# Performance work log

Hardware: AMD Instinct MI355X
Metric: run time of the kernel (lower is better)

Reference implementation:

```python
import jax, jax.numpy as jnp
import numpy as np

N, D_TOK, K = 8192, 256, 16


def knn_idx(xyz, k):
    # squared pairwise distances, diagonal excluded (loop=False)
    sq = jnp.sum(xyz * xyz, axis=-1)                      # [N]
    dist = sq[:, None] - 2.0 * (xyz @ xyz.T) + sq[None, :]  # [N,N]
    dist = dist + jnp.eye(xyz.shape[0], dtype=xyz.dtype) * jnp.asarray(1e10, xyz.dtype)
    _, idx = jax.lax.top_k(-dist, k)                      # [N,k] nearest neighbors j for each target i
    return idx


def edgeconv(x, nbr, W1, b1, W2, b2):
    # EdgeConv message: nn(concat(x_i, x_j - x_i)), aggr = max over neighbors
    n, d = x.shape
    k = nbr.shape[1]
    xi = x[:, None, :]                                    # [N,1,D]
    xj = x[nbr]                                           # [N,k,D] gather
    msg = jnp.concatenate([jnp.broadcast_to(xi, (n, k, d)), xj - xi], axis=-1)  # [N,k,2D]
    h = jax.nn.relu(msg @ W1 + b1) @ W2 + b2              # [N,k,token_dim]
    return jnp.max(h, axis=1)                             # [N,token_dim]


def setup_inputs() -> dict:
    key = jax.random.key(0)
    ks = jax.random.split(key, 10)
    d_in = 2 * (D_TOK + 3)
    s1 = 1.0 / np.sqrt(d_in)
    s2 = 1.0 / np.sqrt(D_TOK)
    return {
        "xyz": jax.random.normal(ks[0], (N, 3), dtype=jnp.float32),
        "feat": jax.random.normal(ks[1], (N, D_TOK), dtype=jnp.float32),
        "W1a": jax.random.normal(ks[2], (d_in, D_TOK), dtype=jnp.float32) * s1,
        "b1a": jnp.zeros((D_TOK,), dtype=jnp.float32),
        "W2a": jax.random.normal(ks[3], (D_TOK, D_TOK), dtype=jnp.float32) * s2,
        "b2a": jnp.zeros((D_TOK,), dtype=jnp.float32),
        "W1b": jax.random.normal(ks[4], (d_in, D_TOK), dtype=jnp.float32) * s1,
        "b1b": jnp.zeros((D_TOK,), dtype=jnp.float32),
        "W2b": jax.random.normal(ks[5], (D_TOK, D_TOK), dtype=jnp.float32) * s2,
        "b2b": jnp.zeros((D_TOK,), dtype=jnp.float32),
    }


def reference(xyz, feat, W1a, b1a, W2a, b2a, W1b, b1b, W2b, b2b):
    nbr = knn_idx(xyz, K)                                 # [N,k], built once, reused by both convs
    x = jnp.concatenate([feat, xyz], axis=-1)             # [N, D_TOK+3]
    x = edgeconv(x, nbr, W1a, b1a, W2a, b2a)              # [N, D_TOK]
    x = jnp.concatenate([x, xyz], axis=-1)                # [N, D_TOK+3]
    x = edgeconv(x, nbr, W1b, b1b, W2b, b2b)              # [N, D_TOK]
    return x
```

## Files before the change

### kernel.cpp

```cpp
#include <hip/hip_runtime.h>
#include <cfloat>

#define N_PTS 8192
#define DTOK 256
#define KNN 16

typedef __attribute__((ext_vector_type(8))) short short8;
typedef __attribute__((ext_vector_type(4))) float float4v;

__device__ inline short f2bf(float f) {
  unsigned u = __float_as_uint(f);
  u += 0x7fffu + ((u >> 16) & 1u);
  return (short)(u >> 16);
}
__device__ inline float bf2f(short h) {
  return __uint_as_float(((unsigned)(unsigned short)h) << 16);
}

__global__ __launch_bounds__(256) void knn_prep_kernel(
    const float* __restrict__ xyz, float4* __restrict__ xyz4) {
  const int i = blockIdx.x * 256 + threadIdx.x;
  float x = xyz[3 * i], y = xyz[3 * i + 1], z = xyz[3 * i + 2];
  float sq = __fadd_rn(__fadd_rn(__fmul_rn(x, x), __fmul_rn(y, y)),
                       __fmul_rn(z, z));
  xyz4[i] = make_float4(x, y, z, sq);
}

__device__ inline float cand_dist(const float4 p, float xi, float yi, float zi,
                                  float sqi, int j, int i) {
  const float dot = fmaf(zi, p.z, fmaf(yi, p.y, __fmul_rn(xi, p.x)));
  float d = __fadd_rn(__fsub_rn(sqi, __fmul_rn(2.0f, dot)), p.w);
  if (j == i) d = __fadd_rn(d, 1e10f);
  return d;
}

__global__ __launch_bounds__(256) void knn_select_kernel(
    const float4* __restrict__ xyz4, int* __restrict__ nbr) {
  const int lane = threadIdx.x & 63;
  const int i = blockIdx.x * 4 + (threadIdx.x >> 6);

  const float4 pi = xyz4[i];
  const float xi = pi.x, yi = pi.y, zi = pi.z, sqi = pi.w;

  float lmin = FLT_MAX;
  #pragma unroll 4
  for (int base = 0; base < N_PTS; base += 64) {
    const int j = base + lane;
    const float4 p = xyz4[j];
    lmin = fminf(lmin, cand_dist(p, xi, yi, zi, sqi, j, i));
  }

  float v = lmin;
  #pragma unroll
  for (int k = 2; k <= 64; k <<= 1) {
    #pragma unroll
    for (int j = k >> 1; j > 0; j >>= 1) {
      const float o = __shfl_xor(v, j, 64);
      const bool up = ((lane & k) == 0);
      const bool lo = ((lane & j) == 0);
      v = (up == lo) ? fminf(v, o) : fmaxf(v, o);
    }
  }
  const float t = __shfl(v, 15, 64);

  float sd = FLT_MAX;
  int sj = 0;
  float s15 = FLT_MAX;

  for (int base = 0; base < N_PTS; base += 64) {
    const int j = base + lane;
    const float4 p = xyz4[j];
    const float d = cand_dist(p, xi, yi, zi, sqi, j, i);

    unsigned long long m = __ballot((d < s15) && (d <= t));
    while (m) {
      const int src = __ffsll(m) - 1;
      m &= m - 1;
      const float dc = __shfl(d, src);
      if (dc < s15) {
        const int jc = base + src;
        const unsigned long long bm = __ballot(sd <= dc) & 0xFFFFull;
        const int pos = (int)__popcll(bm);
        const float pu = __shfl_up(sd, 1);
        const int ju = __shfl_up(sj, 1);
        if (lane < 16) {
          if (lane > pos)        { sd = pu; sj = ju; }
          else if (lane == pos)  { sd = dc; sj = jc; }
        }
        s15 = __shfl(sd, 15);
      }
    }
  }
  if (lane < 16) nbr[i * KNN + lane] = sj;
}

__global__ __launch_bounds__(256) void convert_w_kernel(
    const float* __restrict__ W1, short* __restrict__ bhi,
    short* __restrict__ blo) {
  const int n = blockIdx.x;
  const int k = threadIdx.x;
  const float v = (n < 256) ? W1[k * DTOK + n]
                            : W1[(259 + k) * DTOK + (n - 256)];
  short h = f2bf(v);
  bhi[n * 256 + k] = h;
  blo[n * 256 + k] = f2bf(v - bf2f(h));
}

__global__ __launch_bounds__(256, 2) void pq_gemm_fused_kernel(
    const float* __restrict__ A, const short* __restrict__ Bthi,
    const short* __restrict__ Btlo, const float* __restrict__ xyz,
    const float* __restrict__ W1, const float* __restrict__ b1,
    float* __restrict__ R, float* __restrict__ Q) {
  __shared__ short Ahi[64][32], Alo[64][32];
  __shared__ short Bhi[128][32], Blo[128][32];
  __shared__ float Qs[64][65];
  __shared__ float sx[64][3];
  __shared__ float swz[6][64];
  __shared__ float sb1[64];

  const int tid = threadIdx.x;
  const int lane = tid & 63;
  const int wave = tid >> 6;
  const int l15 = lane & 15;
  const int quad = lane >> 4;
  const int mh = wave & 1;
  const int qh = wave >> 1;
  const int m0 = blockIdx.x * 64;
  const int np0 = blockIdx.y * 64;

  if (tid < 64) {
    sx[tid][0] = xyz[(m0 + tid) * 3];
    sx[tid][1] = xyz[(m0 + tid) * 3 + 1];
    sx[tid][2] = xyz[(m0 + tid) * 3 + 2];
  } else if (tid < 128) {
    int n = tid - 64;
    sb1[n] = b1[np0 + n];
    #pragma unroll
    for (int r = 0; r < 3; ++r) {
      swz[r][n] = W1[(256 + r) * DTOK + np0 + n];
      swz[3 + r][n] = W1[(515 + r) * DTOK + np0 + n];
    }
  }

  float4v acc[2][4];
  #pragma unroll
  for (int mf = 0; mf < 2; ++mf)
    #pragma unroll
    for (int nf = 0; nf < 4; ++nf)
      #pragma unroll
      for (int e = 0; e < 4; ++e) acc[mf][nf][e] = 0.f;

  const int ar = tid >> 2;
  const int ak = (tid & 3) * 8;

  #pragma unroll 1
  for (int kc = 0; kc < 8; ++kc) {
    const int k0 = kc * 32;
    __syncthreads();
    {
      const float* asrc = A + (size_t)(m0 + ar) * 256 + k0 + ak;
      float4 a0 = *(const float4*)asrc;
      float4 a1 = *(const float4*)(asrc + 4);
      float v[8] = {a0.x, a0.y, a0.z, a0.w, a1.x, a1.y, a1.z, a1.w};
      short8 h8, l8;
      #pragma unroll
      for (int e = 0; e < 8; ++e) {
        short h = f2bf(v[e]);
        h8[e] = h;
        l8[e] = f2bf(v[e] - bf2f(h));
      }
      *(short8*)(&Ahi[ar][ak]) = h8;
      *(short8*)(&Alo[ar][ak]) = l8;
    }
    #pragma unroll
    for (int l = 0; l < 4; ++l) {
      const int rem = tid + 256 * (l & 1);
      const int row = rem >> 2;
      const int koff = (rem & 3) * 8;
      const int n = (row < 64) ? (np0 + row) : (256 + np0 + row - 64);
      const short* src = ((l < 2) ? Bthi : Btlo) + (size_t)n * 256 + k0 + koff;
      short8 vv = *(const short8*)src;
      if (l < 2) *(short8*)(&Bhi[row][koff]) = vv;
      else       *(short8*)(&Blo[row][koff]) = vv;
    }
    __syncthreads();

    short8 ah[2], al[2], bh[4], bl[4];
    #pragma unroll
    for (int mf = 0; mf < 2; ++mf) {
      ah[mf] = *(const short8*)(&Ahi[mh * 32 + mf * 16 + l15][quad * 8]);
      al[mf] = *(const short8*)(&Alo[mh * 32 + mf * 16 + l15][quad * 8]);
    }
    #pragma unroll
    for (int nf = 0; nf < 4; ++nf) {
      bh[nf] = *(const short8*)(&Bhi[qh * 64 + nf * 16 + l15][quad * 8]);
      bl[nf] = *(const short8*)(&Blo[qh * 64 + nf * 16 + l15][quad * 8]);
    }
    #pragma unroll
    for (int mf = 0; mf < 2; ++mf)
      #pragma unroll
      for (int nf = 0; nf < 4; ++nf) {
        acc[mf][nf] = __builtin_amdgcn_mfma_f32_16x16x32_bf16(
            ah[mf], bh[nf], acc[mf][nf], 0, 0, 0);
        acc[mf][nf] = __builtin_amdgcn_mfma_f32_16x16x32_bf16(
            ah[mf], bl[nf], acc[mf][nf], 0, 0, 0);
        acc[mf][nf] = __builtin_amdgcn_mfma_f32_16x16x32_bf16(
            al[mf], bh[nf], acc[mf][nf], 0, 0, 0);
      }
  }

  if (qh == 1) {
    #pragma unroll
    for (int mf = 0; mf < 2; ++mf)
      #pragma unroll
      for (int nf = 0; nf < 4; ++nf)
        #pragma unroll
        for (int e = 0; e < 4; ++e) {
          int row = mh * 32 + mf * 16 + quad * 4 + e;
          int col = nf * 16 + l15;
          float q = acc[mf][nf][e] + sx[row][0] * swz[3][col] +
                    sx[row][1] * swz[4][col] + sx[row][2] * swz[5][col];
          Qs[row][col] = q;
          Q[(size_t)(m0 + row) * DTOK + np0 + col] = q;
        }
  }
  __syncthreads();
  if (qh == 0) {
    #pragma unroll
    for (int mf = 0; mf < 2; ++mf)
      #pragma unroll
      for (int nf = 0; nf < 4; ++nf)
        #pragma unroll
        for (int e = 0; e < 4; ++e) {
          int row = mh * 32 + mf * 16 + quad * 4 + e;
          int col = nf * 16 + l15;
          float p = acc[mf][nf][e] + sx[row][0] * swz[0][col] +
                    sx[row][1] * swz[1][col] + sx[row][2] * swz[2][col];
          R[(size_t)(m0 + row) * DTOK + np0 + col] =
              (p + sb1[col]) - Qs[row][col];
        }
  }
}

#define EP 8

__global__ __launch_bounds__(256, 2) void edge_mfma_kernel(
    const float* __restrict__ R, const float* __restrict__ Q,
    const int* __restrict__ nbr, const float* __restrict__ W2,
    const float* __restrict__ b2, float* __restrict__ out,
    int num_groups, int groups_per_block) {
  __shared__ short Hs[EP * KNN * DTOK];
  const int lane = threadIdx.x & 63;
  const int wave = threadIdx.x >> 6;
  const int l15 = lane & 15;
  const int quad = lane >> 4;

  short8 bfr[4][8];
  #pragma unroll
  for (int nt_i = 0; nt_i < 4; ++nt_i) {
    const int n = (wave * 4 + nt_i) * 16 + l15;
    #pragma unroll
    for (int kt = 0; kt < 8; ++kt) {
      short8 f;
      #pragma unroll
      for (int jj = 0; jj < 8; ++jj) {
        int k = kt * 32 + quad * 8 + jj;
        f[jj] = f2bf(W2[k * DTOK + n]);
      }
      bfr[nt_i][kt] = f;
    }
  }

  const int wc8 = lane >> 1;
  const int wsub = (lane & 1) * 4;

  for (int gi = 0; gi < groups_per_block; ++gi) {
    const int g = blockIdx.x + gi * gridDim.x;
    if (g >= num_groups) break;
    const int i0 = g * EP;

    {
      const int ia = i0 + wave * 2;
      const int jr0 = nbr[ia * KNN + l15];
      const int jr1 = nbr[(ia + 1) * KNN + l15];
      const float4 ri0 = ((const float4*)(R + (size_t)ia * DTOK))[lane];
      const float4 ri1 = ((const float4*)(R + (size_t)(ia + 1) * DTOK))[lane];
      #pragma unroll
      for (int pp = 0; pp < 2; ++pp) {
        const float4 ri = pp ? ri1 : ri0;
        const int jr = pp ? jr1 : jr0;
        #pragma unroll
        for (int k = 0; k < KNN; ++k) {
          const int j = __shfl(jr, k, 16);
          const float4 qj = ((const float4*)(Q + (size_t)j * DTOK))[lane];
          const int r = wave * 32 + pp * 16 + k;
          uint2 pk;
          pk.x = ((unsigned)(unsigned short)f2bf(fmaxf(ri.x + qj.x, 0.f))) |
                 (((unsigned)(unsigned short)f2bf(fmaxf(ri.y + qj.y, 0.f))) << 16);
          pk.y = ((unsigned)(unsigned short)f2bf(fmaxf(ri.z + qj.z, 0.f))) |
                 (((unsigned)(unsigned short)f2bf(fmaxf(ri.w + qj.w, 0.f))) << 16);
          *(uint2*)(&Hs[r * DTOK + ((wc8 ^ (r & 7)) << 3) + wsub]) = pk;
        }
      }
    }
    __syncthreads();

    #pragma unroll
    for (int mp = 0; mp < 4; ++mp) {
      float4v acc[2][4];
      #pragma unroll
      for (int mi = 0; mi < 2; ++mi)
        #pragma unroll
        for (int nt_i = 0; nt_i < 4; ++nt_i)
          #pragma unroll
          for (int e = 0; e < 4; ++e) acc[mi][nt_i][e] = 0.f;

      #pragma unroll
      for (int kt = 0; kt < 8; ++kt) {
        const int pc = ((kt * 4 + quad) ^ (l15 & 7)) << 3;
        const short8 a0 = *(const short8*)(
            &Hs[((mp * 2 + 0) * 16 + l15) * DTOK + pc]);
        const short8 a1 = *(const short8*)(
            &Hs[((mp * 2 + 1) * 16 + l15) * DTOK + pc]);
        #pragma unroll
        for (int nt_i = 0; nt_i < 4; ++nt_i) {
          acc[0][nt_i] = __builtin_amdgcn_mfma_f32_16x16x32_bf16(
              a0, bfr[nt_i][kt], acc[0][nt_i], 0, 0, 0);
          acc[1][nt_i] = __builtin_amdgcn_mfma_f32_16x16x32_bf16(
              a1, bfr[nt_i][kt], acc[1][nt_i], 0, 0, 0);
        }
      }

      #pragma unroll
      for (int mi = 0; mi < 2; ++mi) {
        #pragma unroll
        for (int nt_i = 0; nt_i < 4; ++nt_i) {
          float rm = fmaxf(fmaxf(acc[mi][nt_i][0], acc[mi][nt_i][1]),
                           fmaxf(acc[mi][nt_i][2], acc[mi][nt_i][3]));
          rm = fmaxf(rm, __shfl_xor(rm, 16, 64));
          rm = fmaxf(rm, __shfl_xor(rm, 32, 64));
          if (lane < 16) {
            const int i = i0 + mp * 2 + mi;
            const int n = (wave * 4 + nt_i) * 16 + lane;
            out[(size_t)i * DTOK + n] = rm + b2[n];
          }
        }
      }
    }
    __syncthreads();
  }
}

extern "C" void kernel_launch(void* const* d_in, const int* in_sizes, int n_in,
                              void* d_out, int out_size, void* d_ws,
                              size_t ws_size, hipStream_t stream) {
  const float* xyz = (const float*)d_in[0];
  const float* feat = (const float*)d_in[1];
  const float* W1a = (const float*)d_in[2];
  const float* b1a = (const float*)d_in[3];
  const float* W2a = (const float*)d_in[4];
  const float* b2a = (const float*)d_in[5];
  const float* W1b = (const float*)d_in[6];
  const float* b1b = (const float*)d_in[7];
  const float* W2b = (const float*)d_in[8];
  const float* b2b = (const float*)d_in[9];
  float* out = (float*)d_out;

  char* w = (char*)d_ws;
  const size_t SZ_NBR = (size_t)N_PTS * KNN * sizeof(int);
  const size_t MB = 1024 * 1024;
  int* nbr = (int*)w;
  char* w1 = w + SZ_NBR;
  float4* xyz4 = (float4*)w1;
  float* R = (float*)(w1 + 8 * MB);
  float* Q = (float*)(w + SZ_NBR + 16 * MB);
  short* Bthi = (short*)(w + SZ_NBR + 24 * MB);
  short* Btlo = Bthi + 512 * 256;
  float* bufC = out;

  knn_prep_kernel<<<N_PTS / 256, 256, 0, stream>>>(xyz, xyz4);
  knn_select_kernel<<<N_PTS / 4, 256, 0, stream>>>(xyz4, nbr);

  const int num_groups = N_PTS / EP;
  const int nblocks = 512;

  convert_w_kernel<<<512, 256, 0, stream>>>(W1a, Bthi, Btlo);
  pq_gemm_fused_kernel<<<dim3(N_PTS / 64, 4), 256, 0, stream>>>(
      feat, Bthi, Btlo, xyz, W1a, b1a, R, Q);
  edge_mfma_kernel<<<nblocks, 256, 0, stream>>>(R, Q, nbr, W2a, b2a, bufC,
                                                num_groups, 2);

  convert_w_kernel<<<512, 256, 0, stream>>>(W1b, Bthi, Btlo);
  pq_gemm_fused_kernel<<<dim3(N_PTS / 64, 4), 256, 0, stream>>>(
      bufC, Bthi, Btlo, xyz, W1b, b1b, R, Q);
  edge_mfma_kernel<<<nblocks, 256, 0, stream>>>(R, Q, nbr, W2b, b2b, out,
                                                num_groups, 2);
}
```

Baseline: 256.8 us.

## Stage candidate points through double-buffered LDS chunks in kNN select

The kNN selection kernel now loads candidate points cooperatively in 512-point chunks into a double-buffered shared-memory tile shared by the block's four waves, instead of each wave streaming all points from global memory. The next chunk is prefetched into registers while the current one is processed. The second pass also computes eight distances per chunk before running the ballot/insert loop. This cuts redundant global/L2 traffic and exposes ILP, at the cost of block-wide syncs and extra LDS and registers.

```diff
diff --git a/kernel.cpp b/kernel.cpp
--- a/kernel.cpp
+++ b/kernel.cpp
@@ -34,21 +34,50 @@
   return d;
 }
 
+#define KCH 512
+#define NCH (N_PTS / KCH)
+
 __global__ __launch_bounds__(256) void knn_select_kernel(
     const float4* __restrict__ xyz4, int* __restrict__ nbr) {
-  const int lane = threadIdx.x & 63;
-  const int i = blockIdx.x * 4 + (threadIdx.x >> 6);
+  __shared__ float4 cs[2][KCH];
+  const int tid = threadIdx.x;
+  const int lane = tid & 63;
+  const int wave = tid >> 6;
+  const int i = blockIdx.x * 4 + wave;
 
   const float4 pi = xyz4[i];
   const float xi = pi.x, yi = pi.y, zi = pi.z, sqi = pi.w;
 
-  float lmin = FLT_MAX;
-  #pragma unroll 4
-  for (int base = 0; base < N_PTS; base += 64) {
-    const int j = base + lane;
-    const float4 p = xyz4[j];
-    lmin = fminf(lmin, cand_dist(p, xi, yi, zi, sqi, j, i));
-  }
+  float4 p0 = xyz4[tid];
+  float4 p1 = xyz4[tid + 256];
+  cs[0][tid] = p0;
+  cs[0][tid + 256] = p1;
+  __syncthreads();
+
+  float lmin0 = FLT_MAX, lmin1 = FLT_MAX;
+  for (int c = 0; c < NCH; ++c) {
+    const int b = c & 1;
+    if (c < NCH - 1) {
+      p0 = xyz4[(c + 1) * KCH + tid];
+      p1 = xyz4[(c + 1) * KCH + tid + 256];
+    }
+    const int base = c * KCH;
+    #pragma unroll
+    for (int s = 0; s < 8; s += 2) {
+      const float4 q0 = cs[b][s * 64 + lane];
+      const float4 q1 = cs[b][(s + 1) * 64 + lane];
+      lmin0 = fminf(lmin0, cand_dist(q0, xi, yi, zi, sqi,
+                                     base + s * 64 + lane, i));
+      lmin1 = fminf(lmin1, cand_dist(q1, xi, yi, zi, sqi,
+                                     base + (s + 1) * 64 + lane, i));
+    }
+    if (c < NCH - 1) {
+      cs[b ^ 1][tid] = p0;
+      cs[b ^ 1][tid + 256] = p1;
+    }
+    __syncthreads();
+  }
+  const float lmin = fminf(lmin0, lmin1);
 
   float v = lmin;
   #pragma unroll
@@ -67,29 +96,55 @@
   int sj = 0;
   float s15 = FLT_MAX;
 
-  for (int base = 0; base < N_PTS; base += 64) {
-    const int j = base + lane;
-    const float4 p = xyz4[j];
-    const float d = cand_dist(p, xi, yi, zi, sqi, j, i);
-
-    unsigned long long m = __ballot((d < s15) && (d <= t));
-    while (m) {
-      const int src = __ffsll(m) - 1;
-      m &= m - 1;
-      const float dc = __shfl(d, src);
-      if (dc < s15) {
-        const int jc = base + src;
-        const unsigned long long bm = __ballot(sd <= dc) & 0xFFFFull;
-        const int pos = (int)__popcll(bm);
-        const float pu = __shfl_up(sd, 1);
-        const int ju = __shfl_up(sj, 1);
-        if (lane < 16) {
-          if (lane > pos)        { sd = pu; sj = ju; }
-          else if (lane == pos)  { sd = dc; sj = jc; }
-        }
-        s15 = __shfl(sd, 15);
-      }
-    }
+  p0 = xyz4[tid];
+  p1 = xyz4[tid + 256];
+  cs[0][tid] = p0;
+  cs[0][tid + 256] = p1;
+  __syncthreads();
+
+  for (int c = 0; c < NCH; ++c) {
+    const int b = c & 1;
+    if (c < NCH - 1) {
+      p0 = xyz4[(c + 1) * KCH + tid];
+      p1 = xyz4[(c + 1) * KCH + tid + 256];
+    }
+    const int cbase = c * KCH;
+
+    float dd[8];
+    #pragma unroll
+    for (int s = 0; s < 8; ++s) {
+      const float4 q = cs[b][s * 64 + lane];
+      dd[s] = cand_dist(q, xi, yi, zi, sqi, cbase + s * 64 + lane, i);
+    }
+
+    #pragma unroll
+    for (int s = 0; s < 8; ++s) {
+      unsigned long long m = __ballot((dd[s] < s15) && (dd[s] <= t));
+      const int base = cbase + s * 64;
+      while (m) {
+        const int src = __ffsll(m) - 1;
+        m &= m - 1;
+        const float dc = __shfl(dd[s], src);
+        if (dc < s15) {
+          const int jc = base + src;
+          const unsigned long long bm = __ballot(sd <= dc) & 0xFFFFull;
+          const int pos = (int)__popcll(bm);
+          const float pu = __shfl_up(sd, 1);
+          const int ju = __shfl_up(sj, 1);
+          if (lane < 16) {
+            if (lane > pos)        { sd = pu; sj = ju; }
+            else if (lane == pos)  { sd = dc; sj = jc; }
+          }
+          s15 = __shfl(sd, 15);
+        }
+      }
+    }
+
+    if (c < NCH - 1) {
+      cs[b ^ 1][tid] = p0;
+      cs[b ^ 1][tid + 256] = p1;
+    }
+    __syncthreads();
   }
   if (lane < 16) nbr[i * KNN + lane] = sj;
 }
```

Result: faster. 240.2 us (-6.5%).
